# Kernel tuning notes

Measured on AMD Instinct MI355X. Metric: run time of the kernel, lower is better.

## Reference

```python
import jax, jax.numpy as jnp
import numpy as np

N_NODES = 100000
N_EDGES = 600000
D = 128
HEADS = 8
REL = 9
N_GRAPHS = 64


def _relconv(h, coeff, basis, w_loop, b, src, dst, etypes, n_nodes):
    # DGL RelGraphConv, basis regularizer (num_bases == num_rels), sum aggregation,
    # self-loop, bias, relu activation (dropout inactive at eval).
    W = jnp.einsum('rb,bio->rio', coeff, basis)  # [REL, D, D]
    hsrc = h[src]                                # [E, D] gather
    msg = jnp.zeros((hsrc.shape[0], W.shape[2]), h.dtype)
    for r in range(REL):  # small fixed relation set
        msg = msg + jnp.where((etypes == r)[:, None], hsrc @ W[r], 0.0)
    agg = jax.ops.segment_sum(msg, dst, num_segments=n_nodes)
    return jax.nn.relu(agg + h @ w_loop + b)


def _graph_norm(x, seg, n_graphs, w, b, ms):
    # scatter-based per-subgraph normalization (graphNorm)
    counts = jax.ops.segment_sum(jnp.ones((x.shape[0],), x.dtype), seg, num_segments=n_graphs)[:, None]
    mean = jax.ops.segment_sum(x, seg, num_segments=n_graphs) / counts
    sub = x - mean[seg] * ms
    var = jax.ops.segment_sum(sub * sub, seg, num_segments=n_graphs) / counts
    std = jnp.sqrt(var + 1e-6)
    return w * sub / std[seg] + b


def _layer_norm(x, g, b):
    mu = x.mean(-1, keepdims=True)
    v = jnp.mean((x - mu) ** 2, -1, keepdims=True)
    return g * (x - mu) / jnp.sqrt(v + 1e-5) + b


def _forward(h, src, dst, etypes, seg, num_graphs,
             q_coeff, q_basis, q_loop, q_bias,
             k_coeff, k_basis, k_loop, k_bias,
             v_coeff, v_basis, v_loop, v_bias,
             o_w, o_b, gn1_w, gn1_b, gn1_ms, ln1_g, ln1_b,
             gn2_w, gn2_b, gn2_ms, ffn1_w, ffn1_b, ffn2_w, ffn2_b,
             ln2_g, ln2_b):
    n = h.shape[0]
    hn = _graph_norm(h, seg, num_graphs, gn1_w, gn1_b, gn1_ms)
    Q = _relconv(hn, q_coeff, q_basis, q_loop, q_bias, src, dst, etypes, n)
    K = _relconv(hn, k_coeff, k_basis, k_loop, k_bias, src, dst, etypes, n)
    V = _relconv(hn, v_coeff, v_basis, v_loop, v_bias, src, dst, etypes, n)
    dh = D // HEADS
    Qh = Q.reshape(n, HEADS, dh)
    Kh = K.reshape(n, HEADS, dh)
    Vh = V.reshape(n, HEADS, dh)
    # edge dot-product attention: score_e = <K[src], Q[dst]> per head
    score = (Kh[src] * Qh[dst]).sum(-1, keepdims=True)            # [E, H, 1]
    score = jnp.exp(jnp.clip(score / np.float32(np.sqrt(dh)), -10.0, 10.0))
    wV = jax.ops.segment_sum(Vh[src] * score, dst, num_segments=n)  # [N, H, dh]
    z = jax.ops.segment_sum(score, dst, num_segments=n)             # [N, H, 1]
    attn = (wV / (z + 1e-6)).reshape(n, D)
    hO = attn @ o_w + o_b
    h1 = _layer_norm(hO, ln1_g, ln1_b)
    h2 = _graph_norm(h1, seg, num_graphs, gn2_w, gn2_b, gn2_ms)
    h3 = jax.nn.relu(h2 @ ffn1_w + ffn1_b) @ ffn2_w + ffn2_b
    return _layer_norm(h3, ln2_g, ln2_b)


def setup_inputs() -> dict:
    key = jax.random.key(0)
    ks = jax.random.split(key, 32)
    s = np.float32(1.0 / np.sqrt(D))
    inp = {
        'h': jax.random.normal(ks[0], (N_NODES, D), jnp.float32),
        'src': jax.random.randint(ks[1], (N_EDGES,), 0, N_NODES),
        'dst': jax.random.randint(ks[2], (N_EDGES,), 0, N_NODES),
        'etypes': jax.random.randint(ks[3], (N_EDGES,), 0, REL),
        'seg': jnp.sort(jax.random.randint(ks[4], (N_NODES,), 0, N_GRAPHS)),
        'num_graphs': N_GRAPHS,
    }
    def lin(k, i, o):
        return jax.random.normal(k, (i, o), jnp.float32) / np.float32(np.sqrt(i))
    for idx, nm in enumerate(['q', 'k', 'v']):
        base = 5 + idx * 4
        inp[nm + '_coeff'] = jax.random.normal(ks[base], (REL, REL), jnp.float32) / np.float32(np.sqrt(REL))
        inp[nm + '_basis'] = jax.random.normal(ks[base + 1], (REL, D, D), jnp.float32) * s
        inp[nm + '_loop'] = lin(ks[base + 2], D, D)
        inp[nm + '_bias'] = jnp.zeros((D,), jnp.float32)
    inp['o_w'] = lin(ks[17], D, D)
    inp['o_b'] = jnp.zeros((D,), jnp.float32)
    for nm in ['gn1', 'gn2']:
        inp[nm + '_w'] = jnp.ones((D,), jnp.float32)
        inp[nm + '_b'] = jnp.zeros((D,), jnp.float32)
        inp[nm + '_ms'] = jnp.ones((D,), jnp.float32)
    inp['ln1_g'] = jnp.ones((D,), jnp.float32)
    inp['ln1_b'] = jnp.zeros((D,), jnp.float32)
    inp['ln2_g'] = jnp.ones((D,), jnp.float32)
    inp['ln2_b'] = jnp.zeros((D,), jnp.float32)
    inp['ffn1_w'] = lin(ks[18], D, 2 * D)
    inp['ffn1_b'] = jnp.zeros((2 * D,), jnp.float32)
    inp['ffn2_w'] = lin(ks[19], 2 * D, D)
    inp['ffn2_b'] = jnp.zeros((D,), jnp.float32)
    return inp


def reference(h, src, dst, etypes, seg, num_graphs,
              q_coeff, q_basis, q_loop, q_bias,
              k_coeff, k_basis, k_loop, k_bias,
              v_coeff, v_basis, v_loop, v_bias,
              o_w, o_b, gn1_w, gn1_b, gn1_ms, ln1_g, ln1_b,
              gn2_w, gn2_b, gn2_ms, ffn1_w, ffn1_b, ffn2_w, ffn2_b,
              ln2_g, ln2_b):
    return _forward(h, src, dst, etypes, seg, num_graphs,
                    q_coeff, q_basis, q_loop, q_bias,
                    k_coeff, k_basis, k_loop, k_bias,
                    v_coeff, v_basis, v_loop, v_bias,
                    o_w, o_b, gn1_w, gn1_b, gn1_ms, ln1_g, ln1_b,
                    gn2_w, gn2_b, gn2_ms, ffn1_w, ffn1_b, ffn2_w, ffn2_b,
                    ln2_g, ln2_b)
```

## Files before the change

### kernel.cpp

```cpp
#include <hip/hip_runtime.h>
#include <math.h>

#define N_NODES 100000
#define N_EDGES 600000
#define D 128
#define REL 9
#define NG 64
#define NK9 (N_NODES * REL)

typedef float f32x4 __attribute__((ext_vector_type(4)));
typedef _Float16 f16x8 __attribute__((ext_vector_type(8)));
typedef _Float16 h16x2 __attribute__((ext_vector_type(2)));

__device__ __forceinline__ ushort f2h(float x) {
    union { _Float16 h; ushort u; } c; c.h = (_Float16)x; return c.u;
}
__device__ __forceinline__ float h2f(ushort u) {
    union { ushort u; _Float16 h; } c; c.u = u; return (float)c.h;
}

__device__ __forceinline__ void ld16(const ushort* g, ushort* l) {
    __builtin_amdgcn_global_load_lds(
        (const __attribute__((address_space(1))) unsigned int*)g,
        (__attribute__((address_space(3))) unsigned int*)l, 16, 0, 0);
}

__device__ __forceinline__ int lbound(const int* __restrict__ a, int n, int key) {
    int lo = 0, hi = n;
    while (lo < hi) { int mid = (lo + hi) >> 1; if (a[mid] < key) lo = mid + 1; else hi = mid; }
    return lo;
}

__global__ void hist9_kernel(const int* __restrict__ dst, const int* __restrict__ ety,
                             int* __restrict__ cnt9) {
    int e = blockIdx.x * 256 + threadIdx.x;
    if (e < N_EDGES) atomicAdd(&cnt9[dst[e] * REL + ety[e]], 1);
}

__global__ void scan1_8(const int* __restrict__ cnt, int* __restrict__ excl,
                        int* __restrict__ bsum, int n) {
    __shared__ int s[1024];
    int tid = threadIdx.x;
    int base = blockIdx.x * 8192 + tid * 8;
    int v[8]; int sum = 0;
#pragma unroll
    for (int j = 0; j < 8; ++j) { v[j] = (base + j < n) ? cnt[base + j] : 0; sum += v[j]; }
    s[tid] = sum;
    __syncthreads();
    for (int off = 1; off < 1024; off <<= 1) {
        int t = (tid >= off) ? s[tid - off] : 0;
        __syncthreads();
        s[tid] += t;
        __syncthreads();
    }
    int run = s[tid] - sum;
#pragma unroll
    for (int j = 0; j < 8; ++j) { if (base + j < n) excl[base + j] = run; run += v[j]; }
    if (tid == 1023) bsum[blockIdx.x] = s[1023];
}

__global__ void scan2_kernel(int* __restrict__ bsum, int nb) {
    __shared__ int s[128];
    int tid = threadIdx.x;
    int v = (tid < nb) ? bsum[tid] : 0;
    s[tid] = v;
    __syncthreads();
    for (int off = 1; off < 128; off <<= 1) {
        int t = (tid >= off) ? s[tid - off] : 0;
        __syncthreads();
        s[tid] += t;
        __syncthreads();
    }
    if (tid < nb) bsum[tid] = s[tid] - v;
}

__global__ void scan3_8(int* __restrict__ excl, const int* __restrict__ bsum, int n, int total) {
    int base = blockIdx.x * 8192 + threadIdx.x * 8;
    int add = bsum[blockIdx.x];
#pragma unroll
    for (int j = 0; j < 8; ++j) if (base + j < n) excl[base + j] += add;
    if (blockIdx.x == 0 && threadIdx.x == 0) excl[n] = total;
}

__global__ void scatter9_kernel(const int* __restrict__ src, const int* __restrict__ dst,
                                const int* __restrict__ ety, const int* __restrict__ rstart,
                                int* __restrict__ cur9, int* __restrict__ ssrc,
                                int* __restrict__ setp) {
    int e = blockIdx.x * 256 + threadIdx.x;
    if (e < N_EDGES) {
        int t = ety[e];
        int key = dst[e] * REL + t;
        int pos = rstart[key] + atomicAdd(&cur9[key], 1);
        ssrc[pos] = src[e];
        setp[pos] = t;
    }
}

__global__ __launch_bounds__(256)
void gn_stats(const float* __restrict__ x, const int* __restrict__ seg,
              float* __restrict__ gsum, float* __restrict__ gsumsq) {
    __shared__ float redS[8][128];
    __shared__ float redQ[8][128];
    int t = threadIdx.x;
    int c4 = (t & 31) * 4;
    int rr = t >> 5;
    int n0 = blockIdx.x * 128;
    int nend = min(n0 + 128, N_NODES);
    int len = nend - n0;
    int gfirst = seg[n0];
    int glast = seg[nend - 1];
    for (int g = gfirst; g <= glast; ++g) {
        int lo = (g == gfirst) ? n0 : n0 + lbound(seg + n0, len, g);
        int hi = (g == glast) ? nend : n0 + lbound(seg + n0, len, g + 1);
        float s0 = 0.f, s1 = 0.f, s2 = 0.f, s3 = 0.f;
        float q0 = 0.f, q1 = 0.f, q2 = 0.f, q3 = 0.f;
        for (int n = lo + rr; n < hi; n += 8) {
            float4 v = *(const float4*)&x[(size_t)n * D + c4];
            s0 += v.x; q0 += v.x * v.x;
            s1 += v.y; q1 += v.y * v.y;
            s2 += v.z; q2 += v.z * v.z;
            s3 += v.w; q3 += v.w * v.w;
        }
        redS[rr][c4 + 0] = s0; redS[rr][c4 + 1] = s1;
        redS[rr][c4 + 2] = s2; redS[rr][c4 + 3] = s3;
        redQ[rr][c4 + 0] = q0; redQ[rr][c4 + 1] = q1;
        redQ[rr][c4 + 2] = q2; redQ[rr][c4 + 3] = q3;
        __syncthreads();
        if (t < 128) {
            float ts = 0.f, tq = 0.f;
#pragma unroll
            for (int ph = 0; ph < 8; ++ph) { ts += redS[ph][t]; tq += redQ[ph][t]; }
            atomicAdd(&gsum[g * D + t], ts);
            atomicAdd(&gsumsq[g * D + t], tq);
        }
        __syncthreads();
    }
}

__global__ __launch_bounds__(256)
void gn_stats_h(const ushort* __restrict__ x, const int* __restrict__ seg,
                float* __restrict__ gsum, float* __restrict__ gsumsq) {
    __shared__ float redS[8][128];
    __shared__ float redQ[8][128];
    int t = threadIdx.x;
    int c4 = (t & 31) * 4;
    int rr = t >> 5;
    int n0 = blockIdx.x * 128;
    int nend = min(n0 + 128, N_NODES);
    int len = nend - n0;
    int gfirst = seg[n0];
    int glast = seg[nend - 1];
    for (int g = gfirst; g <= glast; ++g) {
        int lo = (g == gfirst) ? n0 : n0 + lbound(seg + n0, len, g);
        int hi = (g == glast) ? nend : n0 + lbound(seg + n0, len, g + 1);
        float s0 = 0.f, s1 = 0.f, s2 = 0.f, s3 = 0.f;
        float q0 = 0.f, q1 = 0.f, q2 = 0.f, q3 = 0.f;
        for (int n = lo + rr; n < hi; n += 8) {
            ushort4 u = *(const ushort4*)&x[(size_t)n * D + c4];
            float v0 = h2f(u.x), v1 = h2f(u.y), v2 = h2f(u.z), v3 = h2f(u.w);
            s0 += v0; q0 += v0 * v0;
            s1 += v1; q1 += v1 * v1;
            s2 += v2; q2 += v2 * v2;
            s3 += v3; q3 += v3 * v3;
        }
        redS[rr][c4 + 0] = s0; redS[rr][c4 + 1] = s1;
        redS[rr][c4 + 2] = s2; redS[rr][c4 + 3] = s3;
        redQ[rr][c4 + 0] = q0; redQ[rr][c4 + 1] = q1;
        redQ[rr][c4 + 2] = q2; redQ[rr][c4 + 3] = q3;
        __syncthreads();
        if (t < 128) {
            float ts = 0.f, tq = 0.f;
#pragma unroll
            for (int ph = 0; ph < 8; ++ph) { ts += redS[ph][t]; tq += redQ[ph][t]; }
            atomicAdd(&gsum[g * D + t], ts);
            atomicAdd(&gsumsq[g * D + t], tq);
        }
        __syncthreads();
    }
}

__global__ void gn_final(const float* __restrict__ gsum, const float* __restrict__ gsumsq,
                         const int* __restrict__ seg, const float* __restrict__ w,
                         const float* __restrict__ b, const float* __restrict__ ms,
                         float* __restrict__ sc, float* __restrict__ off) {
    int g = blockIdx.x, ch = threadIdx.x;
    int lo = lbound(seg, N_NODES, g), hi = lbound(seg, N_NODES, g + 1);
    float cnt = (float)max(hi - lo, 1);
    float mean = gsum[g * D + ch] / cnt;
    float mm = mean * ms[ch];
    float var = gsumsq[g * D + ch] / cnt - 2.f * mm * mean + mm * mm;
    float rstd = rsqrtf(var + 1e-6f);
    float s = w[ch] * rstd;
    sc[g * D + ch] = s;
    off[g * D + ch] = b[ch] - s * mm;
}

__global__ __launch_bounds__(256)
void gn_apply(const float* __restrict__ x, const int* __restrict__ seg,
              const float* __restrict__ sc, const float* __restrict__ off,
              ushort* __restrict__ outhf) {
    int t = blockIdx.x * 256 + threadIdx.x;
    int n = t >> 6;
    if (n >= N_NODES) return;
    int ch = (t & 63) * 2;
    int g = seg[n];
    float2 xv = *(const float2*)&x[(size_t)n * D + ch];
    float2 s2 = *(const float2*)&sc[g * D + ch];
    float2 o2 = *(const float2*)&off[g * D + ch];
    ushort2 o;
    o.x = f2h(s2.x * xv.x + o2.x);
    o.y = f2h(s2.y * xv.y + o2.y);
    *(ushort2*)&outhf[(size_t)n * D + ch] = o;
}

__global__ __launch_bounds__(256)
void gn_apply_h(const ushort* __restrict__ x, const int* __restrict__ seg,
                const float* __restrict__ sc, const float* __restrict__ off,
                ushort* __restrict__ outhf) {
    int t = blockIdx.x * 256 + threadIdx.x;
    int n = t >> 6;
    if (n >= N_NODES) return;
    int ch = (t & 63) * 2;
    int g = seg[n];
    ushort2 xv = *(const ushort2*)&x[(size_t)n * D + ch];
    float2 s2 = *(const float2*)&sc[g * D + ch];
    float2 o2 = *(const float2*)&off[g * D + ch];
    ushort2 o;
    o.x = f2h(s2.x * h2f(xv.x) + o2.x);
    o.y = f2h(s2.y * h2f(xv.y) + o2.y);
    *(ushort2*)&outhf[(size_t)n * D + ch] = o;
}

__global__ void build_bt_qkv3(const float* __restrict__ c0, const float* __restrict__ c1,
                              const float* __restrict__ c2, const float* __restrict__ b0,
                              const float* __restrict__ b1, const float* __restrict__ b2,
                              const float* __restrict__ l0, const float* __restrict__ l1,
                              const float* __restrict__ l2, const float* __restrict__ i0,
                              const float* __restrict__ i1, const float* __restrict__ i2,
                              ushort* __restrict__ Btqkv, float* __restrict__ biasq) {
    int pj = blockIdx.y;
    const float* coeff  = pj == 0 ? c0 : (pj == 1 ? c1 : c2);
    const float* basis  = pj == 0 ? b0 : (pj == 1 ? b1 : b2);
    const float* loop_w = pj == 0 ? l0 : (pj == 1 ? l1 : l2);
    const float* bin    = pj == 0 ? i0 : (pj == 1 ? i1 : i2);
    ushort* Bt = Btqkv + (size_t)pj * 128 * 1280;
    int t = blockIdx.x * 256 + threadIdx.x;
    if (t < 128) biasq[pj * 128 + t] = bin[t];
    if (t >= 128 * 1280) return;
    int o = t / 1280;
    int k = t - o * 1280;
    float v;
    if (k < 128) {
        v = loop_w[k * 128 + o];
    } else {
        int kk = k - 128;
        int r = kk >> 7, i = kk & 127;
        v = 0.f;
#pragma unroll
        for (int b = 0; b < REL; ++b)
            v += coeff[r * REL + b] * basis[((size_t)b * 128 + i) * 128 + o];
    }
    Bt[(size_t)o * 1280 + k] = f2h(v);
}

__global__ void transpose_cast3(const float* __restrict__ o_w, ushort* __restrict__ Bto,
                                const float* __restrict__ f1, ushort* __restrict__ Btf1,
                                const float* __restrict__ f2, ushort* __restrict__ Btf2) {
    int t = blockIdx.x * 256 + threadIdx.x;
    if (t < 16384) {
        int n = t >> 7, k = t & 127;
        Bto[(size_t)n * 128 + k] = f2h(o_w[(size_t)k * 128 + n]);
    } else if (t < 49152) {
        int u = t - 16384;
        int n = u >> 7, k = u & 127;
        Btf1[(size_t)n * 128 + k] = f2h(f1[(size_t)k * 256 + n]);
    } else if (t < 81920) {
        int u = t - 49152;
        int n = u >> 8, k = u & 255;
        Btf2[(size_t)n * 256 + k] = f2h(f2[(size_t)k * 128 + n]);
    }
}

__global__ __launch_bounds__(256)
void s_pass(const ushort* __restrict__ hnhf, const int* __restrict__ ssrc,
            const int* __restrict__ setp, const int* __restrict__ rstart,
            ushort* __restrict__ Ab, int c0, int c1) {
    int n = c0 + ((blockIdx.x * 256 + threadIdx.x) >> 6);
    if (n >= c1) return;
    int lane = threadIdx.x & 63;
    int e0 = rstart[n * REL], e1 = rstart[n * REL + REL];
    h16x2 a0 = (h16x2)0, a1 = (h16x2)0, a2 = (h16x2)0, a3 = (h16x2)0, a4 = (h16x2)0;
    h16x2 a5 = (h16x2)0, a6 = (h16x2)0, a7 = (h16x2)0, a8 = (h16x2)0;
#define ACC(rr, hv) switch (rr) { \
        case 0: a0 += hv; break; case 1: a1 += hv; break; case 2: a2 += hv; break; \
        case 3: a3 += hv; break; case 4: a4 += hv; break; case 5: a5 += hv; break; \
        case 6: a6 += hv; break; case 7: a7 += hv; break; default: a8 += hv; break; }
    int e = e0;
    for (; e + 4 <= e1; e += 4) {
        int s0 = ssrc[e], s1 = ssrc[e + 1], s2 = ssrc[e + 2], s3 = ssrc[e + 3];
        int r0 = __builtin_amdgcn_readfirstlane(setp[e]);
        int r1 = __builtin_amdgcn_readfirstlane(setp[e + 1]);
        int r2 = __builtin_amdgcn_readfirstlane(setp[e + 2]);
        int r3 = __builtin_amdgcn_readfirstlane(setp[e + 3]);
        h16x2 hv0 = *(const h16x2*)&hnhf[(size_t)s0 * D + 2 * lane];
        h16x2 hv1 = *(const h16x2*)&hnhf[(size_t)s1 * D + 2 * lane];
        h16x2 hv2 = *(const h16x2*)&hnhf[(size_t)s2 * D + 2 * lane];
        h16x2 hv3 = *(const h16x2*)&hnhf[(size_t)s3 * D + 2 * lane];
        ACC(r0, hv0)
        ACC(r1, hv1)
        ACC(r2, hv2)
        ACC(r3, hv3)
    }
    for (; e < e1; ++e) {
        int s0 = ssrc[e];
        int r0 = __builtin_amdgcn_readfirstlane(setp[e]);
        h16x2 hv0 = *(const h16x2*)&hnhf[(size_t)s0 * D + 2 * lane];
        ACC(r0, hv0)
    }
#undef ACC
    ushort* arow = Ab + (size_t)(n - c0) * 1152;
#define ST(r) *(h16x2*)&arow[r * 128 + 2 * lane] = a##r;
    ST(0) ST(1) ST(2) ST(3) ST(4) ST(5) ST(6) ST(7) ST(8)
#undef ST
}

__global__ __launch_bounds__(512)
void mfma_gemm384(const ushort* __restrict__ A1, const ushort* __restrict__ Ab, int M,
                  const ushort* __restrict__ Bt, const float* __restrict__ bias,
                  ushort* __restrict__ Cout) {
    __shared__ ushort As[128 * 64];
    __shared__ ushort Bs[384 * 64];
    const int tid = threadIdx.x;
    const int lane = tid & 63;
    const int wave = tid >> 6;
    const int wm = wave & 1, wn = wave >> 1;
    const int quad = lane >> 4, l16 = lane & 15;
    const int row0 = blockIdx.x * 128;

    const ushort* sA1[2];
    const ushort* sA2[2];
#pragma unroll
    for (int i = 0; i < 2; ++i) {
        int rs = (wave * 2 + i) * 8 + (lane >> 3);
        int kg = (lane & 7) ^ (rs & 7);
        int ra = row0 + rs; if (ra >= M) ra = M - 1;
        sA1[i] = A1 + (size_t)ra * 128 + kg * 8;
        sA2[i] = Ab + (size_t)ra * 1152 + kg * 8;
    }
    const ushort* sB[6];
#pragma unroll
    for (int i = 0; i < 6; ++i) {
        int rs = (wave * 6 + i) * 8 + (lane >> 3);
        int kg = (lane & 7) ^ (rs & 7);
        sB[i] = Bt + (size_t)rs * 1280 + kg * 8;
    }

    f32x4 acc[4][6];
#pragma unroll
    for (int i = 0; i < 4; ++i)
#pragma unroll
        for (int j = 0; j < 6; ++j) acc[i][j] = (f32x4){0.f, 0.f, 0.f, 0.f};

    for (int kc = 0; kc < 1280; kc += 64) {
#pragma unroll
        for (int i = 0; i < 6; ++i) ld16(sB[i] + kc, &Bs[(wave * 6 + i) * 512]);
#pragma unroll
        for (int i = 0; i < 2; ++i) {
            const ushort* as = (kc < 128) ? (sA1[i] + kc) : (sA2[i] + (kc - 128));
            ld16(as, &As[(wave * 2 + i) * 512]);
        }
        __syncthreads();
#pragma unroll
        for (int h = 0; h < 2; ++h) {
            f16x8 af[4], bf[6];
#pragma unroll
            for (int i = 0; i < 4; ++i) {
                int r = wm * 64 + i * 16 + l16;
                af[i] = *(const f16x8*)&As[r * 64 + (((h * 4 + quad) ^ (r & 7)) * 8)];
            }
#pragma unroll
            for (int j = 0; j < 6; ++j) {
                int c = wn * 96 + j * 16 + l16;
                bf[j] = *(const f16x8*)&Bs[c * 64 + (((h * 4 + quad) ^ (c & 7)) * 8)];
            }
#pragma unroll
            for (int i = 0; i < 4; ++i)
#pragma unroll
                for (int j = 0; j < 6; ++j)
                    acc[i][j] = __builtin_amdgcn_mfma_f32_16x16x32_f16(af[i], bf[j], acc[i][j], 0, 0, 0);
        }
        __syncthreads();
    }

#pragma unroll
    for (int i = 0; i < 4; ++i) {
        int gr0 = wm * 64 + i * 16 + quad * 4 + row0;
#pragma unroll
        for (int r = 0; r < 4; ++r) {
            int gr = gr0 + r;
            if (gr >= M) continue;
#pragma unroll
            for (int j = 0; j < 6; ++j) {
                int gcol = wn * 96 + j * 16 + l16;
                float v = acc[i][j][r] + bias[gcol];
                v = fmaxf(v, 0.f);
                Cout[(size_t)gr * 384 + gcol] = f2h(v);
            }
        }
    }
}

template<bool SPLITA, bool RELU, bool F16OUT>
__global__ __launch_bounds__(256, 3)
void mfma_gemm(const ushort* __restrict__ A1, const ushort* __restrict__ A2, int lda2, int M,
               const ushort* __restrict__ Bt, int K,
               const float* __restrict__ bias, void* __restrict__ Cout, int ldc) {
    __shared__ ushort As[128 * 64];
    __shared__ ushort Bs[128 * 64];
    const int tid = threadIdx.x;
    const int lane = tid & 63;
    const int wave = tid >> 6;
    const int wm = wave & 1, wn = wave >> 1;
    const int quad = lane >> 4, l16 = lane & 15;
    const int col0 = blockIdx.x * 128, row0 = blockIdx.y * 128;

    const ushort* sA1[4];
    const ushort* sA2[4];
    const ushort* sB[4];
#pragma unroll
    for (int i = 0; i < 4; ++i) {
        int rs = (wave * 4 + i) * 8 + (lane >> 3);
        int kg = (lane & 7) ^ (rs & 7);
        int ra = row0 + rs; if (ra >= M) ra = M - 1;
        sA1[i] = SPLITA ? (A1 + (size_t)ra * 128 + kg * 8) : nullptr;
        sA2[i] = A2 + (size_t)ra * lda2 + kg * 8;
        sB[i]  = Bt + (size_t)(col0 + rs) * K + kg * 8;
    }

    f32x4 acc[4][4];
#pragma unroll
    for (int i = 0; i < 4; ++i)
#pragma unroll
        for (int j = 0; j < 4; ++j) acc[i][j] = (f32x4){0.f, 0.f, 0.f, 0.f};

    for (int kc = 0; kc < K; kc += 64) {
#pragma unroll
        for (int i = 0; i < 4; ++i) {
            const ushort* as = (SPLITA && kc < 128) ? (sA1[i] + kc) : (sA2[i] + (SPLITA ? kc - 128 : kc));
            ld16(as, &As[(wave * 4 + i) * 512]);
            ld16(sB[i] + kc, &Bs[(wave * 4 + i) * 512]);
        }
        __syncthreads();
#pragma unroll
        for (int h = 0; h < 2; ++h) {
            f16x8 af[4], bf[4];
#pragma unroll
            for (int i = 0; i < 4; ++i) {
                int r = wm * 64 + i * 16 + l16;
                af[i] = *(const f16x8*)&As[r * 64 + (((h * 4 + quad) ^ (r & 7)) * 8)];
                int c = wn * 64 + i * 16 + l16;
                bf[i] = *(const f16x8*)&Bs[c * 64 + (((h * 4 + quad) ^ (c & 7)) * 8)];
            }
#pragma unroll
            for (int i = 0; i < 4; ++i)
#pragma unroll
                for (int j = 0; j < 4; ++j)
                    acc[i][j] = __builtin_amdgcn_mfma_f32_16x16x32_f16(af[i], bf[j], acc[i][j], 0, 0, 0);
        }
        __syncthreads();
    }

#pragma unroll
    for (int i = 0; i < 4; ++i) {
        int gr0 = row0 + wm * 64 + i * 16 + quad * 4;
#pragma unroll
        for (int r = 0; r < 4; ++r) {
            int grow = gr0 + r;
            if (grow >= M) continue;
#pragma unroll
            for (int j = 0; j < 4; ++j) {
                int gcol = col0 + wn * 64 + j * 16 + l16;
                float v = acc[i][j][r] + bias[gcol];
                if (RELU) v = fmaxf(v, 0.f);
                if (F16OUT) ((ushort*)Cout)[(size_t)grow * ldc + gcol] = f2h(v);
                else        ((float*)Cout)[(size_t)grow * ldc + gcol] = v;
            }
        }
    }
}

template<bool F16OUT>
__global__ __launch_bounds__(256, 3)
void mfma_gemm_ln(const ushort* __restrict__ A, int lda, int M,
                  const ushort* __restrict__ Bt, int K,
                  const float* __restrict__ bias, const float* __restrict__ lng,
                  const float* __restrict__ lnb, void* __restrict__ Cout) {
    __shared__ ushort As[128 * 64];
    __shared__ ushort Bs[128 * 64];
    __shared__ float rsum[2][128];
    __shared__ float rsq[2][128];
    const int tid = threadIdx.x;
    const int lane = tid & 63;
    const int wave = tid >> 6;
    const int wm = wave & 1, wn = wave >> 1;
    const int quad = lane >> 4, l16 = lane & 15;
    const int row0 = blockIdx.y * 128;

    const ushort* sA[4];
    const ushort* sB[4];
#pragma unroll
    for (int i = 0; i < 4; ++i) {
        int rs = (wave * 4 + i) * 8 + (lane >> 3);
        int kg = (lane & 7) ^ (rs & 7);
        int ra = row0 + rs; if (ra >= M) ra = M - 1;
        sA[i] = A + (size_t)ra * lda + kg * 8;
        sB[i] = Bt + (size_t)rs * K + kg * 8;
    }

    f32x4 acc[4][4];
#pragma unroll
    for (int i = 0; i < 4; ++i)
#pragma unroll
        for (int j = 0; j < 4; ++j) acc[i][j] = (f32x4){0.f, 0.f, 0.f, 0.f};

    for (int kc = 0; kc < K; kc += 64) {
#pragma unroll
        for (int i = 0; i < 4; ++i) {
            ld16(sA[i] + kc, &As[(wave * 4 + i) * 512]);
            ld16(sB[i] + kc, &Bs[(wave * 4 + i) * 512]);
        }
        __syncthreads();
#pragma unroll
        for (int h = 0; h < 2; ++h) {
            f16x8 af[4], bf[4];
#pragma unroll
            for (int i = 0; i < 4; ++i) {
                int r = wm * 64 + i * 16 + l16;
                af[i] = *(const f16x8*)&As[r * 64 + (((h * 4 + quad) ^ (r & 7)) * 8)];
                int c = wn * 64 + i * 16 + l16;
                bf[i] = *(const f16x8*)&Bs[c * 64 + (((h * 4 + quad) ^ (c & 7)) * 8)];
            }
#pragma unroll
            for (int i = 0; i < 4; ++i)
#pragma unroll
                for (int j = 0; j < 4; ++j)
                    acc[i][j] = __builtin_amdgcn_mfma_f32_16x16x32_f16(af[i], bf[j], acc[i][j], 0, 0, 0);
        }
        __syncthreads();
    }

#pragma unroll
    for (int i = 0; i < 4; ++i) {
#pragma unroll
        for (int r = 0; r < 4; ++r) {
            float s = 0.f, q = 0.f;
#pragma unroll
            for (int j = 0; j < 4; ++j) {
                float v = acc[i][j][r] + bias[wn * 64 + j * 16 + l16];
                s += v; q += v * v;
            }
            s += __shfl_xor(s, 1); q += __shfl_xor(q, 1);
            s += __shfl_xor(s, 2); q += __shfl_xor(q, 2);
            s += __shfl_xor(s, 4); q += __shfl_xor(q, 4);
            s += __shfl_xor(s, 8); q += __shfl_xor(q, 8);
            if (l16 == 0) {
                int row = wm * 64 + i * 16 + quad * 4 + r;
                rsum[wn][row] = s;
                rsq[wn][row] = q;
            }
        }
    }
    __syncthreads();

#pragma unroll
    for (int i = 0; i < 4; ++i) {
#pragma unroll
        for (int r = 0; r < 4; ++r) {
            int row = wm * 64 + i * 16 + quad * 4 + r;
            int grow = row0 + row;
            if (grow >= M) continue;
            float tot = rsum[0][row] + rsum[1][row];
            float tq  = rsq[0][row] + rsq[1][row];
            float mu = tot * (1.f / 128.f);
            float var = tq * (1.f / 128.f) - mu * mu;
            float rstd = rsqrtf(var + 1e-5f);
#pragma unroll
            for (int j = 0; j < 4; ++j) {
                int gcol = wn * 64 + j * 16 + l16;
                float v = acc[i][j][r] + bias[gcol];
                float o = lng[gcol] * (v - mu) * rstd + lnb[gcol];
                if (F16OUT) ((ushort*)Cout)[(size_t)grow * 128 + gcol] = f2h(o);
                else        ((float*)Cout)[(size_t)grow * 128 + gcol] = o;
            }
        }
    }
}

__global__ __launch_bounds__(256)
void attn_kernel(const ushort* __restrict__ C, const int* __restrict__ ssrc,
                 const int* __restrict__ rstart, ushort* __restrict__ attnhf) {
    int n = (blockIdx.x * 256 + threadIdx.x) >> 6;
    if (n >= N_NODES) return;
    int lane = threadIdx.x & 63;
    h16x2 qh = *(const h16x2*)&C[(size_t)n * 384 + 2 * lane];
    int e0 = rstart[n * REL], e1 = rstart[n * REL + REL];
    float wvx = 0.f, wvy = 0.f, z = 0.f;
    int e = e0;
    for (; e + 8 <= e1; e += 8) {
        int s[8];
#pragma unroll
        for (int j = 0; j < 8; ++j) s[j] = ssrc[e + j];
        h16x2 kk[8], vv[8];
#pragma unroll
        for (int j = 0; j < 8; ++j) kk[j] = *(const h16x2*)&C[(size_t)s[j] * 384 + 128 + 2 * lane];
#pragma unroll
        for (int j = 0; j < 8; ++j) vv[j] = *(const h16x2*)&C[(size_t)s[j] * 384 + 256 + 2 * lane];
        float d[8];
#pragma unroll
        for (int j = 0; j < 8; ++j) d[j] = __builtin_amdgcn_fdot2(kk[j], qh, 0.f, false);
#pragma unroll
        for (int j = 0; j < 8; ++j) d[j] += __shfl_xor(d[j], 1);
#pragma unroll
        for (int j = 0; j < 8; ++j) d[j] += __shfl_xor(d[j], 2);
#pragma unroll
        for (int j = 0; j < 8; ++j) d[j] += __shfl_xor(d[j], 4);
#pragma unroll
        for (int j = 0; j < 8; ++j) {
            float sc = __expf(fminf(fmaxf(d[j] * 0.25f, -10.f), 10.f));
            wvx += sc * (float)vv[j].x;
            wvy += sc * (float)vv[j].y;
            z += sc;
        }
    }
    for (; e + 4 <= e1; e += 4) {
        int s0 = ssrc[e], s1 = ssrc[e + 1], s2 = ssrc[e + 2], s3 = ssrc[e + 3];
        h16x2 k0 = *(const h16x2*)&C[(size_t)s0 * 384 + 128 + 2 * lane];
        h16x2 k1 = *(const h16x2*)&C[(size_t)s1 * 384 + 128 + 2 * lane];
        h16x2 k2 = *(const h16x2*)&C[(size_t)s2 * 384 + 128 + 2 * lane];
        h16x2 k3 = *(const h16x2*)&C[(size_t)s3 * 384 + 128 + 2 * lane];
        h16x2 v0 = *(const h16x2*)&C[(size_t)s0 * 384 + 256 + 2 * lane];
        h16x2 v1 = *(const h16x2*)&C[(size_t)s1 * 384 + 256 + 2 * lane];
        h16x2 v2 = *(const h16x2*)&C[(size_t)s2 * 384 + 256 + 2 * lane];
        h16x2 v3 = *(const h16x2*)&C[(size_t)s3 * 384 + 256 + 2 * lane];
        float d0 = __builtin_amdgcn_fdot2(k0, qh, 0.f, false);
        float d1 = __builtin_amdgcn_fdot2(k1, qh, 0.f, false);
        float d2 = __builtin_amdgcn_fdot2(k2, qh, 0.f, false);
        float d3 = __builtin_amdgcn_fdot2(k3, qh, 0.f, false);
        d0 += __shfl_xor(d0, 1); d1 += __shfl_xor(d1, 1);
        d2 += __shfl_xor(d2, 1); d3 += __shfl_xor(d3, 1);
        d0 += __shfl_xor(d0, 2); d1 += __shfl_xor(d1, 2);
        d2 += __shfl_xor(d2, 2); d3 += __shfl_xor(d3, 2);
        d0 += __shfl_xor(d0, 4); d1 += __shfl_xor(d1, 4);
        d2 += __shfl_xor(d2, 4); d3 += __shfl_xor(d3, 4);
        float sc0 = __expf(fminf(fmaxf(d0 * 0.25f, -10.f), 10.f));
        float sc1 = __expf(fminf(fmaxf(d1 * 0.25f, -10.f), 10.f));
        float sc2 = __expf(fminf(fmaxf(d2 * 0.25f, -10.f), 10.f));
        float sc3 = __expf(fminf(fmaxf(d3 * 0.25f, -10.f), 10.f));
        wvx += sc0 * (float)v0.x + sc1 * (float)v1.x;
        wvy += sc0 * (float)v0.y + sc1 * (float)v1.y;
        wvx += sc2 * (float)v2.x + sc3 * (float)v3.x;
        wvy += sc2 * (float)v2.y + sc3 * (float)v3.y;
        z += sc0 + sc1 + sc2 + sc3;
    }
    for (; e < e1; ++e) {
        int s0 = ssrc[e];
        h16x2 k0 = *(const h16x2*)&C[(size_t)s0 * 384 + 128 + 2 * lane];
        h16x2 v0 = *(const h16x2*)&C[(size_t)s0 * 384 + 256 + 2 * lane];
        float d0 = __builtin_amdgcn_fdot2(k0, qh, 0.f, false);
        d0 += __shfl_xor(d0, 1);
        d0 += __shfl_xor(d0, 2);
        d0 += __shfl_xor(d0, 4);
        float sc0 = __expf(fminf(fmaxf(d0 * 0.25f, -10.f), 10.f));
        wvx += sc0 * (float)v0.x;
        wvy += sc0 * (float)v0.y;
        z += sc0;
    }
    float inv = 1.f / (z + 1e-6f);
    ushort2 o;
    o.x = f2h(wvx * inv);
    o.y = f2h(wvy * inv);
    *(ushort2*)&attnhf[(size_t)n * D + 2 * lane] = o;
}

extern "C" void kernel_launch(void* const* d_in, const int* in_sizes, int n_in,
                              void* d_out, int out_size, void* d_ws, size_t ws_size,
                              hipStream_t stream) {
    (void)in_sizes; (void)n_in; (void)out_size;
    const float* h     = (const float*)d_in[0];
    const int*   src   = (const int*)d_in[1];
    const int*   dst   = (const int*)d_in[2];
    const int*   ety   = (const int*)d_in[3];
    const int*   seg   = (const int*)d_in[4];
    const float* coeffs[3] = {(const float*)d_in[6],  (const float*)d_in[10], (const float*)d_in[14]};
    const float* bases [3] = {(const float*)d_in[7],  (const float*)d_in[11], (const float*)d_in[15]};
    const float* loops [3] = {(const float*)d_in[8],  (const float*)d_in[12], (const float*)d_in[16]};
    const float* pbias [3] = {(const float*)d_in[9],  (const float*)d_in[13], (const float*)d_in[17]};
    const float* o_w   = (const float*)d_in[18];
    const float* o_b   = (const float*)d_in[19];
    const float* gn1_w = (const float*)d_in[20];
    const float* gn1_b = (const float*)d_in[21];
    const float* gn1_ms= (const float*)d_in[22];
    const float* gn2_w = (const float*)d_in[23];
    const float* gn2_b = (const float*)d_in[24];
    const float* gn2_ms= (const float*)d_in[25];
    const float* ln1_g = (const float*)d_in[26];
    const float* ln1_b = (const float*)d_in[27];
    const float* ln2_g = (const float*)d_in[28];
    const float* ln2_b = (const float*)d_in[29];
    const float* ffn1_w= (const float*)d_in[30];
    const float* ffn1_b= (const float*)d_in[31];
    const float* ffn2_w= (const float*)d_in[32];
    const float* ffn2_b= (const float*)d_in[33];

    char* p = (char*)d_ws;
    auto take = [&](size_t bytes) { char* r = p; p += (bytes + 255) & ~(size_t)255; return r; };
    int*    cnt9   = (int*)take((size_t)NK9 * 2 * 4);
    int*    cur9   = cnt9 + NK9;
    int*    rstart = (int*)take((size_t)(NK9 + 8) * 4);
    int*    bsum   = (int*)take(512);
    int*    ssrc   = (int*)take((size_t)N_EDGES * 4);
    int*    setp   = (int*)take((size_t)N_EDGES * 4);
    float*  gsum   = (float*)take((size_t)NG * D * 4 * 2);
    float*  gsumsq = gsum + NG * D;
    float*  gsc    = (float*)take((size_t)NG * D * 4);
    float*  goff   = (float*)take((size_t)NG * D * 4);
    ushort* Btqkv  = (ushort*)take((size_t)384 * 1280 * 2);
    float*  biasq  = (float*)take(384 * 4);
    ushort* Bto    = (ushort*)take((size_t)128 * 128 * 2);
    ushort* Btf1   = (ushort*)take((size_t)256 * 128 * 2);
    ushort* Btf2   = (ushort*)take((size_t)128 * 256 * 2);
    ushort* hnhf   = (ushort*)take((size_t)N_NODES * D * 2);
    ushort* attnhf = (ushort*)take((size_t)N_NODES * D * 2);
    ushort* h1hf   = (ushort*)take((size_t)N_NODES * D * 2);
    ushort* Cqkv   = (ushort*)take((size_t)N_NODES * 384 * 2);
    size_t used = (size_t)(p - (char*)d_ws);
    size_t avail = (ws_size > used) ? ws_size - used : 0;
    int NC = 1;
    if (avail < (size_t)N_NODES * 1152 * 2) NC = 4;
    if (NC == 4 && avail < ((size_t)(N_NODES / 4 + 1) * 1152 * 2)) NC = 8;
    ushort* Ab = (ushort*)p;
    const int chunk = (N_NODES + NC - 1) / NC;

    ushort* gn2hf  = Cqkv;
    ushort* ffn1hf = (ushort*)((char*)Cqkv + 25600000);

    const int EB = (N_EDGES + 255) / 256;
    const int KB = (NK9 + 8191) / 8192;
    const int WB = (N_NODES * 64 + 255) / 256;
    const int GB = (N_NODES + 127) / 128;
    const int RB = (N_NODES + 127) / 128;

    hipMemsetAsync(cnt9, 0, (size_t)NK9 * 8, stream);
    hist9_kernel<<<EB, 256, 0, stream>>>(dst, ety, cnt9);
    scan1_8<<<KB, 1024, 0, stream>>>(cnt9, rstart, bsum, NK9);
    scan2_kernel<<<1, 128, 0, stream>>>(bsum, KB);
    scan3_8<<<KB, 1024, 0, stream>>>(rstart, bsum, NK9, N_EDGES);
    scatter9_kernel<<<EB, 256, 0, stream>>>(src, dst, ety, rstart, cur9, ssrc, setp);

    build_bt_qkv3<<<dim3(640, 3), 256, 0, stream>>>(
        coeffs[0], coeffs[1], coeffs[2], bases[0], bases[1], bases[2],
        loops[0], loops[1], loops[2], pbias[0], pbias[1], pbias[2], Btqkv, biasq);
    transpose_cast3<<<320, 256, 0, stream>>>(o_w, Bto, ffn1_w, Btf1, ffn2_w, Btf2);

    hipMemsetAsync(gsum, 0, (size_t)NG * D * 8, stream);
    gn_stats<<<GB, 256, 0, stream>>>(h, seg, gsum, gsumsq);
    gn_final<<<NG, 128, 0, stream>>>(gsum, gsumsq, seg, gn1_w, gn1_b, gn1_ms, gsc, goff);
    gn_apply<<<WB, 256, 0, stream>>>(h, seg, gsc, goff, hnhf);

    for (int c = 0; c < NC; ++c) {
        int c0 = c * chunk;
        int c1 = min(N_NODES, c0 + chunk);
        int rows = c1 - c0;
        if (rows <= 0) break;
        s_pass<<<(rows + 3) / 4, 256, 0, stream>>>(hnhf, ssrc, setp, rstart, Ab, c0, c1);
        mfma_gemm384<<<(rows + 127) / 128, 512, 0, stream>>>(
            hnhf + (size_t)c0 * 128, Ab, rows, Btqkv, biasq, Cqkv + (size_t)c0 * 384);
    }

    attn_kernel<<<WB, 256, 0, stream>>>(Cqkv, ssrc, rstart, attnhf);

    mfma_gemm_ln<true><<<dim3(1, RB), 256, 0, stream>>>(
        attnhf, 128, N_NODES, Bto, 128, o_b, ln1_g, ln1_b, h1hf);

    hipMemsetAsync(gsum, 0, (size_t)NG * D * 8, stream);
    gn_stats_h<<<GB, 256, 0, stream>>>(h1hf, seg, gsum, gsumsq);
    gn_final<<<NG, 128, 0, stream>>>(gsum, gsumsq, seg, gn2_w, gn2_b, gn2_ms, gsc, goff);
    gn_apply_h<<<WB, 256, 0, stream>>>(h1hf, seg, gsc, goff, gn2hf);

    mfma_gemm<false, true, true><<<dim3(2, RB), 256, 0, stream>>>(
        nullptr, gn2hf, 128, N_NODES, Btf1, 128, ffn1_b, ffn1hf, 256);
    mfma_gemm_ln<false><<<dim3(1, RB), 256, 0, stream>>>(
        ffn1hf, 256, N_NODES, Btf2, 256, ffn2_b, ln2_g, ln2_b, (float*)d_out);
}
```

Baseline: 743.3 us.

## Fuse FFN1 GEMM, ReLU, FFN2 GEMM and LayerNorm into one kernel

Replaces the two-kernel FFN (an up-projection GEMM that writes a 256-wide f16 intermediate to global memory, then a GEMM+LayerNorm that reads it back) with a single 512-thread kernel. Each block computes its 128-row tile of the ReLU intermediate straight into swizzled LDS and runs the down-projection and LayerNorm from there. This removes the global write and read of the N×256 intermediate and one kernel launch. The cost is about 100KB of dynamic LDS per block, which lowers occupancy, and the block count drops from 2×RB to RB for the first GEMM.

New measurement: 750.8 us. Within noise of the previous version (+1.0%).

```diff
diff --git a/kernel.cpp b/kernel.cpp
--- a/kernel.cpp
+++ b/kernel.cpp
@@ -410,85 +410,6 @@
     }
 }
 
-template<bool SPLITA, bool RELU, bool F16OUT>
-__global__ __launch_bounds__(256, 3)
-void mfma_gemm(const ushort* __restrict__ A1, const ushort* __restrict__ A2, int lda2, int M,
-               const ushort* __restrict__ Bt, int K,
-               const float* __restrict__ bias, void* __restrict__ Cout, int ldc) {
-    __shared__ ushort As[128 * 64];
-    __shared__ ushort Bs[128 * 64];
-    const int tid = threadIdx.x;
-    const int lane = tid & 63;
-    const int wave = tid >> 6;
-    const int wm = wave & 1, wn = wave >> 1;
-    const int quad = lane >> 4, l16 = lane & 15;
-    const int col0 = blockIdx.x * 128, row0 = blockIdx.y * 128;
-
-    const ushort* sA1[4];
-    const ushort* sA2[4];
-    const ushort* sB[4];
-#pragma unroll
-    for (int i = 0; i < 4; ++i) {
-        int rs = (wave * 4 + i) * 8 + (lane >> 3);
-        int kg = (lane & 7) ^ (rs & 7);
-        int ra = row0 + rs; if (ra >= M) ra = M - 1;
-        sA1[i] = SPLITA ? (A1 + (size_t)ra * 128 + kg * 8) : nullptr;
-        sA2[i] = A2 + (size_t)ra * lda2 + kg * 8;
-        sB[i]  = Bt + (size_t)(col0 + rs) * K + kg * 8;
-    }
-
-    f32x4 acc[4][4];
-#pragma unroll
-    for (int i = 0; i < 4; ++i)
-#pragma unroll
-        for (int j = 0; j < 4; ++j) acc[i][j] = (f32x4){0.f, 0.f, 0.f, 0.f};
-
-    for (int kc = 0; kc < K; kc += 64) {
-#pragma unroll
-        for (int i = 0; i < 4; ++i) {
-            const ushort* as = (SPLITA && kc < 128) ? (sA1[i] + kc) : (sA2[i] + (SPLITA ? kc - 128 : kc));
-            ld16(as, &As[(wave * 4 + i) * 512]);
-            ld16(sB[i] + kc, &Bs[(wave * 4 + i) * 512]);
-        }
-        __syncthreads();
-#pragma unroll
-        for (int h = 0; h < 2; ++h) {
-            f16x8 af[4], bf[4];
-#pragma unroll
-            for (int i = 0; i < 4; ++i) {
-                int r = wm * 64 + i * 16 + l16;
-                af[i] = *(const f16x8*)&As[r * 64 + (((h * 4 + quad) ^ (r & 7)) * 8)];
-                int c = wn * 64 + i * 16 + l16;
-                bf[i] = *(const f16x8*)&Bs[c * 64 + (((h * 4 + quad) ^ (c & 7)) * 8)];
-            }
-#pragma unroll
-            for (int i = 0; i < 4; ++i)
-#pragma unroll
-                for (int j = 0; j < 4; ++j)
-                    acc[i][j] = __builtin_amdgcn_mfma_f32_16x16x32_f16(af[i], bf[j], acc[i][j], 0, 0, 0);
-        }
-        __syncthreads();
-    }
-
-#pragma unroll
-    for (int i = 0; i < 4; ++i) {
-        int gr0 = row0 + wm * 64 + i * 16 + quad * 4;
-#pragma unroll
-        for (int r = 0; r < 4; ++r) {
-            int grow = gr0 + r;
-            if (grow >= M) continue;
-#pragma unroll
-            for (int j = 0; j < 4; ++j) {
-                int gcol = col0 + wn * 64 + j * 16 + l16;
-                float v = acc[i][j][r] + bias[gcol];
-                if (RELU) v = fmaxf(v, 0.f);
-                if (F16OUT) ((ushort*)Cout)[(size_t)grow * ldc + gcol] = f2h(v);
-                else        ((float*)Cout)[(size_t)grow * ldc + gcol] = v;
-            }
-        }
-    }
-}
-
 template<bool F16OUT>
 __global__ __launch_bounds__(256, 3)
 void mfma_gemm_ln(const ushort* __restrict__ A, int lda, int M,
@@ -591,6 +512,183 @@
                 float o = lng[gcol] * (v - mu) * rstd + lnb[gcol];
                 if (F16OUT) ((ushort*)Cout)[(size_t)grow * 128 + gcol] = f2h(o);
                 else        ((float*)Cout)[(size_t)grow * 128 + gcol] = o;
+            }
+        }
+    }
+}
+
+__global__ __launch_bounds__(512)
+void ffn_fused(const ushort* __restrict__ A, int M,
+               const ushort* __restrict__ B1t, const float* __restrict__ b1,
+               const ushort* __restrict__ B2t, const float* __restrict__ b2,
+               const float* __restrict__ lng, const float* __restrict__ lnb,
+               float* __restrict__ Cout) {
+    extern __shared__ ushort sh[];
+    ushort* As   = sh;
+    ushort* Bs   = sh + 128 * 64;
+    ushort* C1s  = sh + 128 * 64 + 256 * 64;
+    float*  rsum = (float*)(C1s + 128 * 256);
+    float*  rsq  = rsum + 4 * 128;
+    const int tid = threadIdx.x;
+    const int lane = tid & 63;
+    const int wave = tid >> 6;
+    const int quad = lane >> 4, l16 = lane & 15;
+    const int row0 = blockIdx.x * 128;
+
+    {
+        const int wm = wave & 1, wn = wave >> 1;
+        const ushort* sA[2];
+#pragma unroll
+        for (int i = 0; i < 2; ++i) {
+            int rs = (wave * 2 + i) * 8 + (lane >> 3);
+            int kg = (lane & 7) ^ (rs & 7);
+            int ra = row0 + rs; if (ra >= M) ra = M - 1;
+            sA[i] = A + (size_t)ra * 128 + kg * 8;
+        }
+        const ushort* sB[4];
+#pragma unroll
+        for (int i = 0; i < 4; ++i) {
+            int rs = (wave * 4 + i) * 8 + (lane >> 3);
+            int kg = (lane & 7) ^ (rs & 7);
+            sB[i] = B1t + (size_t)rs * 128 + kg * 8;
+        }
+        f32x4 acc[4][4];
+#pragma unroll
+        for (int i = 0; i < 4; ++i)
+#pragma unroll
+            for (int j = 0; j < 4; ++j) acc[i][j] = (f32x4){0.f, 0.f, 0.f, 0.f};
+
+        for (int kc = 0; kc < 128; kc += 64) {
+#pragma unroll
+            for (int i = 0; i < 4; ++i) ld16(sB[i] + kc, &Bs[(wave * 4 + i) * 512]);
+#pragma unroll
+            for (int i = 0; i < 2; ++i) ld16(sA[i] + kc, &As[(wave * 2 + i) * 512]);
+            __syncthreads();
+#pragma unroll
+            for (int h = 0; h < 2; ++h) {
+                f16x8 af[4], bf[4];
+#pragma unroll
+                for (int i = 0; i < 4; ++i) {
+                    int r = wm * 64 + i * 16 + l16;
+                    af[i] = *(const f16x8*)&As[r * 64 + (((h * 4 + quad) ^ (r & 7)) * 8)];
+                }
+#pragma unroll
+                for (int j = 0; j < 4; ++j) {
+                    int c = wn * 64 + j * 16 + l16;
+                    bf[j] = *(const f16x8*)&Bs[c * 64 + (((h * 4 + quad) ^ (c & 7)) * 8)];
+                }
+#pragma unroll
+                for (int i = 0; i < 4; ++i)
+#pragma unroll
+                    for (int j = 0; j < 4; ++j)
+                        acc[i][j] = __builtin_amdgcn_mfma_f32_16x16x32_f16(af[i], bf[j], acc[i][j], 0, 0, 0);
+            }
+            __syncthreads();
+        }
+
+#pragma unroll
+        for (int i = 0; i < 4; ++i) {
+            int lr0 = wm * 64 + i * 16 + quad * 4;
+#pragma unroll
+            for (int r = 0; r < 4; ++r) {
+                int row = lr0 + r;
+                int rw = row & 7;
+#pragma unroll
+                for (int j = 0; j < 4; ++j) {
+                    int cbase = j * 16 + l16;
+                    int kg = cbase >> 3;
+                    float v = acc[i][j][r] + b1[wn * 64 + cbase];
+                    v = fmaxf(v, 0.f);
+                    C1s[row * 256 + wn * 64 + ((kg ^ rw) * 8) + (cbase & 7)] = f2h(v);
+                }
+            }
+        }
+    }
+    __syncthreads();
+
+    {
+        const int wm = wave & 1, wn = wave >> 1;
+        const ushort* sB[2];
+#pragma unroll
+        for (int i = 0; i < 2; ++i) {
+            int rs = (wave * 2 + i) * 8 + (lane >> 3);
+            int kg = (lane & 7) ^ (rs & 7);
+            sB[i] = B2t + (size_t)rs * 256 + kg * 8;
+        }
+        f32x4 acc[4][2];
+#pragma unroll
+        for (int i = 0; i < 4; ++i)
+#pragma unroll
+            for (int j = 0; j < 2; ++j) acc[i][j] = (f32x4){0.f, 0.f, 0.f, 0.f};
+
+        for (int kc = 0; kc < 256; kc += 64) {
+#pragma unroll
+            for (int i = 0; i < 2; ++i) ld16(sB[i] + kc, &Bs[(wave * 2 + i) * 512]);
+            __syncthreads();
+#pragma unroll
+            for (int h = 0; h < 2; ++h) {
+                f16x8 af[4], bf[2];
+#pragma unroll
+                for (int i = 0; i < 4; ++i) {
+                    int r = wm * 64 + i * 16 + l16;
+                    af[i] = *(const f16x8*)&C1s[r * 256 + kc + (((h * 4 + quad) ^ (r & 7)) * 8)];
+                }
+#pragma unroll
+                for (int j = 0; j < 2; ++j) {
+                    int c = wn * 32 + j * 16 + l16;
+                    bf[j] = *(const f16x8*)&Bs[c * 64 + (((h * 4 + quad) ^ (c & 7)) * 8)];
+                }
+#pragma unroll
+                for (int i = 0; i < 4; ++i)
+#pragma unroll
+                    for (int j = 0; j < 2; ++j)
+                        acc[i][j] = __builtin_amdgcn_mfma_f32_16x16x32_f16(af[i], bf[j], acc[i][j], 0, 0, 0);
+            }
+            __syncthreads();
+        }
+
+#pragma unroll
+        for (int i = 0; i < 4; ++i) {
+#pragma unroll
+            for (int r = 0; r < 4; ++r) {
+                float s = 0.f, q = 0.f;
+#pragma unroll
+                for (int j = 0; j < 2; ++j) {
+                    float v = acc[i][j][r] + b2[wn * 32 + j * 16 + l16];
+                    s += v; q += v * v;
+                }
+                s += __shfl_xor(s, 1); q += __shfl_xor(q, 1);
+                s += __shfl_xor(s, 2); q += __shfl_xor(q, 2);
+                s += __shfl_xor(s, 4); q += __shfl_xor(q, 4);
+                s += __shfl_xor(s, 8); q += __shfl_xor(q, 8);
+                if (l16 == 0) {
+                    int row = wm * 64 + i * 16 + quad * 4 + r;
+                    rsum[wn * 128 + row] = s;
+                    rsq[wn * 128 + row] = q;
+                }
+            }
+        }
+        __syncthreads();
+
+#pragma unroll
+        for (int i = 0; i < 4; ++i) {
+#pragma unroll
+            for (int r = 0; r < 4; ++r) {
+                int row = wm * 64 + i * 16 + quad * 4 + r;
+                int grow = row0 + row;
+                if (grow >= M) continue;
+                float tot = rsum[row] + rsum[128 + row] + rsum[256 + row] + rsum[384 + row];
+                float tq  = rsq[row] + rsq[128 + row] + rsq[256 + row] + rsq[384 + row];
+                float mu = tot * (1.f / 128.f);
+                float var = tq * (1.f / 128.f) - mu * mu;
+                float rstd = rsqrtf(var + 1e-5f);
+#pragma unroll
+                for (int j = 0; j < 2; ++j) {
+                    int gcol = wn * 32 + j * 16 + l16;
+                    float v = acc[i][j][r] + b2[gcol];
+                    float o = lng[gcol] * (v - mu) * rstd + lnb[gcol];
+                    Cout[(size_t)grow * 128 + gcol] = o;
+                }
             }
         }
     }
@@ -742,7 +840,6 @@
     const int chunk = (N_NODES + NC - 1) / NC;
 
     ushort* gn2hf  = Cqkv;
-    ushort* ffn1hf = (ushort*)((char*)Cqkv + 25600000);
 
     const int EB = (N_EDGES + 255) / 256;
     const int KB = (NK9 + 8191) / 8192;
@@ -787,8 +884,8 @@
     gn_final<<<NG, 128, 0, stream>>>(gsum, gsumsq, seg, gn2_w, gn2_b, gn2_ms, gsc, goff);
     gn_apply_h<<<WB, 256, 0, stream>>>(h1hf, seg, gsc, goff, gn2hf);
 
-    mfma_gemm<false, true, true><<<dim3(2, RB), 256, 0, stream>>>(
-        nullptr, gn2hf, 128, N_NODES, Btf1, 128, ffn1_b, ffn1hf, 256);
-    mfma_gemm_ln<false><<<dim3(1, RB), 256, 0, stream>>>(
-        ffn1hf, 256, N_NODES, Btf2, 256, ffn2_b, ln2_g, ln2_b, (float*)d_out);
-}
+    const int FFN_LDS = (128 * 64 + 256 * 64 + 128 * 256) * 2 + 4 * 128 * 4 * 2;
+    hipFuncSetAttribute((const void*)ffn_fused, hipFuncAttributeMaxDynamicSharedMemorySize, FFN_LDS);
+    ffn_fused<<<RB, 512, FFN_LDS, stream>>>(
+        gn2hf, N_NODES, Btf1, ffn1_b, Btf2, ffn2_b, ln2_g, ln2_b, (float*)d_out);
+}
```
